# Performance work log

Hardware: AMD Instinct MI355X
Metric: run time of the kernel (lower is better)

Reference implementation:

```python
import jax, jax.numpy as jnp
import numpy as np

N, L, D_MODEL, N_HEADS = 2, 2048, 512, 8

def setup_inputs() -> dict:
    key = jax.random.key(0)
    x = jax.random.normal(key, (N, L, D_MODEL), dtype=jnp.float32)
    return {"input_data": x}

def reference(input_data):
    n, l, _ = input_data.shape
    h = N_HEADS
    d = D_MODEL // h  # head dim
    # Q = K = V = reshaped input (the Linear projections are unused in the original forward)
    q = input_data.reshape(n, l, h, d)
    k = q
    v = q
    scale = 1.0 / jnp.sqrt(jnp.float32(d))
    # scores: [n, h, l, s]
    scores = jnp.einsum('nlhd,nshd->nhls', q, k)
    attn_weights = jax.nn.softmax(scale * scores, axis=-1)
    # updated values: [n, l, h, d]
    updated_v = jnp.einsum('nhls,nshd->nlhd', attn_weights, v)
    out = updated_v.reshape(n, l, h * d)
    # attn returned as mean over heads: permute nhls -> nlhs, mean over h -> [n, l, s]
    attn = jnp.transpose(attn_weights, (0, 2, 1, 3)).mean(axis=-2)
    return (out, attn)
```

## Files before the change

### kernel.cpp

```cpp
#include <hip/hip_runtime.h>

#define NBATCH 2
#define SEQ    2048
#define DMODEL 512
#define NH     8
#define HDIM   64
#define SCALE  0.125f

typedef __attribute__((ext_vector_type(8))) short bf16x8;
typedef __attribute__((ext_vector_type(4))) float f32x4;

__device__ __forceinline__ unsigned short f2bf(float f) {
    union { float f; unsigned u; } v; v.f = f;
    unsigned r = v.u + 0x7FFFu + ((v.u >> 16) & 1u);
    return (unsigned short)(r >> 16);
}

__device__ __forceinline__ void pack4(unsigned short* dst, float4 v) {
    unsigned long long pk = (unsigned long long)f2bf(v.x)
        | ((unsigned long long)f2bf(v.y) << 16)
        | ((unsigned long long)f2bf(v.z) << 32)
        | ((unsigned long long)f2bf(v.w) << 48);
    *(unsigned long long*)dst = pk;
}

__device__ __forceinline__ bf16x8 pack8(float4 a, float4 b) {
    bf16x8 r;
    r[0]=(short)f2bf(a.x); r[1]=(short)f2bf(a.y); r[2]=(short)f2bf(a.z); r[3]=(short)f2bf(a.w);
    r[4]=(short)f2bf(b.x); r[5]=(short)f2bf(b.y); r[6]=(short)f2bf(b.z); r[7]=(short)f2bf(b.w);
    return r;
}

__device__ __forceinline__ void gld_lds16(const unsigned short* g, unsigned short* l) {
    __builtin_amdgcn_global_load_lds(
        (const __attribute__((address_space(1))) unsigned int*)(const void*)g,
        (__attribute__((address_space(3))) unsigned int*)(void*)l, 16, 0, 0);
}

__global__ __launch_bounds__(256) void prep_kernel(const float* __restrict__ x,
                                                   unsigned short* __restrict__ xb,
                                                   unsigned short* __restrict__ xt) {
    __shared__ unsigned short Tb[64][72];
    const int bid = blockIdx.x;
    const int n = bid >> 8, h = (bid >> 5) & 7, st = bid & 31;
    const int s0 = st * 64;
    const int t = threadIdx.x;
    {
        const int s = t >> 2, d0 = (t & 3) * 16;
        const float* xp = x + ((size_t)(n*SEQ + s0 + s))*DMODEL + h*HDIM + d0;
        #pragma unroll
        for (int i = 0; i < 4; ++i) pack4(&Tb[s][d0 + 4*i], *(const float4*)(xp + 4*i));
    }
    __syncthreads();
    {
        const int s = t >> 2, d0 = (t & 3) * 16;
        unsigned short* bp = xb + ((size_t)(n*SEQ + s0 + s))*DMODEL + h*HDIM + d0;
        *(bf16x8*)bp       = *(const bf16x8*)&Tb[s][d0];
        *(bf16x8*)(bp + 8) = *(const bf16x8*)&Tb[s][d0 + 8];
    }
    {
        const int d = t >> 2, c0 = (t & 3) * 16;
        bf16x8 v0, v1;
        #pragma unroll
        for (int j = 0; j < 8; ++j) {
            v0[j] = (short)Tb[c0 + j][d];
            v1[j] = (short)Tb[c0 + 8 + j][d];
        }
        unsigned short* tp = xt + ((size_t)((n*NH + h)*HDIM + d))*SEQ + s0 + c0;
        *(bf16x8*)tp       = v0;
        *(bf16x8*)(tp + 8) = v1;
    }
}

__global__ __launch_bounds__(256) void out_kernel3(const unsigned short* __restrict__ xb,
                                                   const unsigned short* __restrict__ xt,
                                                   float* __restrict__ out,
                                                   float* __restrict__ rho) {
    __shared__ unsigned short Kb[2][64*64];
    __shared__ unsigned short Vt[2][64*64];
    __shared__ unsigned short pb[64][72];

    const int i   = blockIdx.x;
    const int bid = (i & 7) * 64 + (i >> 3);
    const int n = bid >> 8, h = (bid >> 5) & 7, lt = bid & 31;
    const int l0 = lt * 64;
    const int tid = threadIdx.x;
    const int wv = tid >> 6, lane = tid & 63;
    const int lr = lane & 15, lg = lane >> 4;

    const unsigned short* qp = xb + ((size_t)(n*SEQ + l0 + wv*16 + lr))*DMODEL + h*HDIM + lg*8;
    const bf16x8 a0 = *(const bf16x8*)qp;
    const bf16x8 a1 = *(const bf16x8*)(qp + 32);

    const int srow8  = wv*8 + (lane >> 3);
    const int schunk = lane & 7;
    const unsigned short* kbase = xb + (size_t)(n*SEQ)*DMODEL + h*HDIM;
    const unsigned short* vbase = xt + ((size_t)(n*NH + h)*HDIM)*SEQ;

    auto stage = [&](int buf, int s0) {
        #pragma unroll
        for (int it = 0; it < 2; ++it) {
            const int row = it*32 + srow8;
            const int gc  = schunk ^ (row & 7);
            gld_lds16(kbase + (size_t)(s0 + row)*DMODEL + gc*8,
                      &Kb[buf][it*2048 + wv*512]);
        }
        #pragma unroll
        for (int it = 0; it < 2; ++it) {
            const int d  = it*32 + srow8;
            const int gc = schunk ^ (d & 7);
            gld_lds16(vbase + (size_t)d*SEQ + s0 + gc*8,
                      &Vt[buf][it*2048 + wv*512]);
        }
    };

    f32x4 ov0 = {0.f,0.f,0.f,0.f}, ov1 = {0.f,0.f,0.f,0.f};
    f32x4 ov2 = {0.f,0.f,0.f,0.f}, ov3 = {0.f,0.f,0.f,0.f};
    float rs[4] = {0.f,0.f,0.f,0.f};

    stage(0, 0);
    __syncthreads();
    int cur = 0;

    for (int c = 0; c < 32; ++c) {
        if (c < 31) stage(cur ^ 1, (c + 1) * 64);

        const int c0 = (lg ^ (lr & 7)) << 3;
        #pragma unroll
        for (int ct = 0; ct < 4; ++ct) {
            const unsigned short* kr = &Kb[cur][(ct*16 + lr)*64];
            bf16x8 b0 = *(const bf16x8*)&kr[c0];
            bf16x8 b1 = *(const bf16x8*)&kr[c0 ^ 32];
            f32x4 acc = {0.f,0.f,0.f,0.f};
            acc = __builtin_amdgcn_mfma_f32_16x16x32_bf16(a0, b0, acc, 0,0,0);
            acc = __builtin_amdgcn_mfma_f32_16x16x32_bf16(a1, b1, acc, 0,0,0);
            #pragma unroll
            for (int r = 0; r < 4; ++r) {
                const float e = __expf(acc[r] * SCALE);
                rs[r] += e;
                pb[wv*16 + lg*4 + r][ct*16 + lr] = f2bf(e);
            }
        }
        #pragma unroll
        for (int ks = 0; ks < 2; ++ks) {
            const bf16x8 pa = *(const bf16x8*)&pb[wv*16 + lr][ks*32 + lg*8];
            const int cc = ((ks*4 + lg) ^ (lr & 7)) << 3;
            const bf16x8 w0 = *(const bf16x8*)&Vt[cur][( 0 + lr)*64 + cc];
            const bf16x8 w1 = *(const bf16x8*)&Vt[cur][(16 + lr)*64 + cc];
            const bf16x8 w2 = *(const bf16x8*)&Vt[cur][(32 + lr)*64 + cc];
            const bf16x8 w3 = *(const bf16x8*)&Vt[cur][(48 + lr)*64 + cc];
            ov0 = __builtin_amdgcn_mfma_f32_16x16x32_bf16(pa, w0, ov0, 0,0,0);
            ov1 = __builtin_amdgcn_mfma_f32_16x16x32_bf16(pa, w1, ov1, 0,0,0);
            ov2 = __builtin_amdgcn_mfma_f32_16x16x32_bf16(pa, w2, ov2, 0,0,0);
            ov3 = __builtin_amdgcn_mfma_f32_16x16x32_bf16(pa, w3, ov3, 0,0,0);
        }
        __syncthreads();
        cur ^= 1;
    }

    #pragma unroll
    for (int r = 0; r < 4; ++r) {
        float s = rs[r];
        s += __shfl_xor(s, 1, 16);
        s += __shfl_xor(s, 2, 16);
        s += __shfl_xor(s, 4, 16);
        s += __shfl_xor(s, 8, 16);
        rs[r] = s;
    }
    const int row0 = l0 + wv*16 + lg*4;
    if (lr == 0) {
        #pragma unroll
        for (int r = 0; r < 4; ++r)
            rho[(size_t)(n*NH + h)*SEQ + row0 + r] = rs[r];
    }
    #pragma unroll
    for (int r = 0; r < 4; ++r) {
        const float iv = 1.f / rs[r];
        float* op = out + ((size_t)(n*SEQ + row0 + r))*DMODEL + h*HDIM + lr;
        op[0]  = ov0[r] * iv;
        op[16] = ov1[r] * iv;
        op[32] = ov2[r] * iv;
        op[48] = ov3[r] * iv;
    }
}

__global__ __launch_bounds__(256) void mean_kernel3(const unsigned short* __restrict__ xb,
                                                    const float* __restrict__ rho,
                                                    float* __restrict__ attn) {
    __shared__ unsigned short Qb[2][64*64];
    __shared__ unsigned short Kb[2][64*64];
    __shared__ float invb[NH][64];

    const int i   = blockIdx.x;
    const int bid = (i & 7) * 256 + (i >> 3);
    const int n = bid >> 10, lt = (bid >> 5) & 31, st = bid & 31;
    const int l0 = lt * 64, s0 = st * 64;
    const int tid = threadIdx.x;
    const int wv = tid >> 6, lane = tid & 63;
    const int lr = lane & 15, lg = lane >> 4;

    for (int j = tid; j < NH*64; j += 256) {
        const int hh = j >> 6, row = j & 63;
        invb[hh][row] = 0.125f / rho[(size_t)(n*NH + hh)*SEQ + l0 + row];
    }

    const int srow8  = wv*8 + (lane >> 3);
    const int schunk = lane & 7;

    auto stage = [&](int buf, int h) {
        #pragma unroll
        for (int it = 0; it < 2; ++it) {
            const int row = it*32 + srow8;
            const int gc  = schunk ^ (row & 7);
            gld_lds16(xb + ((size_t)(n*SEQ + l0 + row))*DMODEL + h*HDIM + gc*8,
                      &Qb[buf][it*2048 + wv*512]);
        }
        #pragma unroll
        for (int it = 0; it < 2; ++it) {
            const int row = it*32 + srow8;
            const int gc  = schunk ^ (row & 7);
            gld_lds16(xb + ((size_t)(n*SEQ + s0 + row))*DMODEL + h*HDIM + gc*8,
                      &Kb[buf][it*2048 + wv*512]);
        }
    };

    float mean[4][4];
    #pragma unroll
    for (int ct = 0; ct < 4; ++ct)
        #pragma unroll
        for (int r = 0; r < 4; ++r) mean[ct][r] = 0.f;

    stage(0, 0);
    __syncthreads();
    int cur = 0;

    for (int h = 0; h < NH; ++h) {
        if (h < NH-1) stage(cur ^ 1, h + 1);

        const int qrow = wv*16 + lr;
        const int c0 = (lg ^ (lr & 7)) << 3;
        const bf16x8 a0 = *(const bf16x8*)&Qb[cur][qrow*64 + c0];
        const bf16x8 a1 = *(const bf16x8*)&Qb[cur][qrow*64 + (c0 ^ 32)];
        #pragma unroll
        for (int ct = 0; ct < 4; ++ct) {
            const unsigned short* kr = &Kb[cur][(ct*16 + lr)*64];
            bf16x8 b0 = *(const bf16x8*)&kr[c0];
            bf16x8 b1 = *(const bf16x8*)&kr[c0 ^ 32];
            f32x4 acc = {0.f,0.f,0.f,0.f};
            acc = __builtin_amdgcn_mfma_f32_16x16x32_bf16(a0, b0, acc, 0,0,0);
            acc = __builtin_amdgcn_mfma_f32_16x16x32_bf16(a1, b1, acc, 0,0,0);
            #pragma unroll
            for (int r = 0; r < 4; ++r)
                mean[ct][r] += __expf(acc[r] * SCALE) * invb[h][wv*16 + lg*4 + r];
        }
        __syncthreads();
        cur ^= 1;
    }

    #pragma unroll
    for (int ct = 0; ct < 4; ++ct)
        #pragma unroll
        for (int r = 0; r < 4; ++r)
            attn[((size_t)(n*SEQ + l0 + wv*16 + lg*4 + r))*SEQ + s0 + ct*16 + lr]
                = mean[ct][r];
}

__global__ __launch_bounds__(256) void fb_out_kernel(const float* __restrict__ x,
                                                     float* __restrict__ out,
                                                     float* __restrict__ rho) {
    __shared__ unsigned short Kbuf[128][72];
    __shared__ unsigned short vT[64][136];
    __shared__ unsigned short pbuf[64][136];
    const int bid = blockIdx.x;
    const int n  = bid >> 8, h = (bid >> 5) & 7, lt = bid & 31;
    const int l0 = lt * 64;
    const int tid = threadIdx.x;
    const int wv  = tid >> 6, lane = tid & 63;
    const int lr  = lane & 15, lg = lane >> 4;
    const float* qp = x + ((size_t)(n*SEQ + l0 + wv*16 + lr))*DMODEL + h*HDIM + lg*8;
    const bf16x8 a0 = pack8(*(const float4*)qp,      *(const float4*)(qp+4));
    const bf16x8 a1 = pack8(*(const float4*)(qp+32), *(const float4*)(qp+36));
    f32x4 ov0 = {0.f,0.f,0.f,0.f}, ov1 = {0.f,0.f,0.f,0.f};
    f32x4 ov2 = {0.f,0.f,0.f,0.f}, ov3 = {0.f,0.f,0.f,0.f};
    float rs[4] = {0.f,0.f,0.f,0.f};
    for (int s0 = 0; s0 < SEQ; s0 += 128) {
        __syncthreads();
        {
            const int srow = tid >> 1, dbase = (tid & 1) * 32;
            const float* kp = x + ((size_t)(n*SEQ + s0 + srow))*DMODEL + h*HDIM + dbase;
            #pragma unroll
            for (int i = 0; i < 8; ++i) {
                float4 v = *(const float4*)(kp + 4*i);
                pack4(&Kbuf[srow][dbase + 4*i], v);
                const int d = dbase + 4*i;
                vT[d+0][srow] = f2bf(v.x); vT[d+1][srow] = f2bf(v.y);
                vT[d+2][srow] = f2bf(v.z); vT[d+3][srow] = f2bf(v.w);
            }
        }
        __syncthreads();
        #pragma unroll
        for (int ct = 0; ct < 8; ++ct) {
            const unsigned short* bp = &Kbuf[ct*16 + lr][lg*8];
            bf16x8 b0 = *(const bf16x8*)bp;
            bf16x8 b1 = *(const bf16x8*)(bp + 32);
            f32x4 acc = {0.f,0.f,0.f,0.f};
            acc = __builtin_amdgcn_mfma_f32_16x16x32_bf16(a0, b0, acc, 0,0,0);
            acc = __builtin_amdgcn_mfma_f32_16x16x32_bf16(a1, b1, acc, 0,0,0);
            #pragma unroll
            for (int r = 0; r < 4; ++r) {
                const float e = __expf(acc[r] * SCALE);
                rs[r] += e;
                pbuf[wv*16 + lg*4 + r][ct*16 + lr] = f2bf(e);
            }
        }
        __syncthreads();
        #pragma unroll
        for (int ks = 0; ks < 4; ++ks) {
            bf16x8 pa = *(const bf16x8*)&pbuf[wv*16 + lr][ks*32 + lg*8];
            bf16x8 v0 = *(const bf16x8*)&vT[ 0 + lr][ks*32 + lg*8];
            bf16x8 v1 = *(const bf16x8*)&vT[16 + lr][ks*32 + lg*8];
            bf16x8 v2 = *(const bf16x8*)&vT[32 + lr][ks*32 + lg*8];
            bf16x8 v3 = *(const bf16x8*)&vT[48 + lr][ks*32 + lg*8];
            ov0 = __builtin_amdgcn_mfma_f32_16x16x32_bf16(pa, v0, ov0, 0,0,0);
            ov1 = __builtin_amdgcn_mfma_f32_16x16x32_bf16(pa, v1, ov1, 0,0,0);
            ov2 = __builtin_amdgcn_mfma_f32_16x16x32_bf16(pa, v2, ov2, 0,0,0);
            ov3 = __builtin_amdgcn_mfma_f32_16x16x32_bf16(pa, v3, ov3, 0,0,0);
        }
    }
    #pragma unroll
    for (int r = 0; r < 4; ++r) {
        float s = rs[r];
        s += __shfl_xor(s, 1, 16); s += __shfl_xor(s, 2, 16);
        s += __shfl_xor(s, 4, 16); s += __shfl_xor(s, 8, 16);
        rs[r] = s;
    }
    const int row0 = l0 + wv*16 + lg*4;
    if (lr == 0) {
        #pragma unroll
        for (int r = 0; r < 4; ++r)
            rho[(size_t)(n*NH + h)*SEQ + row0 + r] = rs[r];
    }
    #pragma unroll
    for (int r = 0; r < 4; ++r) {
        const float iv = 1.f / rs[r];
        float* op = out + ((size_t)(n*SEQ + row0 + r))*DMODEL + h*HDIM + lr;
        op[0] = ov0[r]*iv; op[16] = ov1[r]*iv; op[32] = ov2[r]*iv; op[48] = ov3[r]*iv;
    }
}

__global__ __launch_bounds__(256) void fb_mean_kernel(const float* __restrict__ x,
                                                      const float* __restrict__ rho,
                                                      float* __restrict__ attn) {
    __shared__ unsigned short Qb[64][72];
    __shared__ unsigned short Kb[128][72];
    __shared__ float          invb[64];
    const int bid = blockIdx.x;
    const int n  = bid >> 9, lt = (bid >> 4) & 31, st = bid & 15;
    const int l0 = lt * 64, s0 = st * 128;
    const int tid = threadIdx.x;
    const int wv  = tid >> 6, lane = tid & 63;
    const int lr  = lane & 15, lg = lane >> 4;
    float mean[8][4];
    #pragma unroll
    for (int ct = 0; ct < 8; ++ct)
        #pragma unroll
        for (int r = 0; r < 4; ++r) mean[ct][r] = 0.f;
    for (int h = 0; h < NH; ++h) {
        __syncthreads();
        {
            const int qrow = tid >> 2, qd = (tid & 3) * 16;
            const float* qp = x + ((size_t)(n*SEQ + l0 + qrow))*DMODEL + h*HDIM + qd;
            #pragma unroll
            for (int i = 0; i < 4; ++i)
                pack4(&Qb[qrow][qd + 4*i], *(const float4*)(qp + 4*i));
        }
        {
            const int srow = tid >> 1, dbase = (tid & 1) * 32;
            const float* kp = x + ((size_t)(n*SEQ + s0 + srow))*DMODEL + h*HDIM + dbase;
            #pragma unroll
            for (int i = 0; i < 8; ++i)
                pack4(&Kb[srow][dbase + 4*i], *(const float4*)(kp + 4*i));
        }
        if (tid < 64)
            invb[tid] = 0.125f / rho[(size_t)(n*NH + h)*SEQ + l0 + tid];
        __syncthreads();
        const unsigned short* ap = &Qb[wv*16 + lr][lg*8];
        const bf16x8 a0 = *(const bf16x8*)ap;
        const bf16x8 a1 = *(const bf16x8*)(ap + 32);
        #pragma unroll
        for (int ct = 0; ct < 8; ++ct) {
            const unsigned short* bp = &Kb[ct*16 + lr][lg*8];
            bf16x8 b0 = *(const bf16x8*)bp;
            bf16x8 b1 = *(const bf16x8*)(bp + 32);
            f32x4 acc = {0.f,0.f,0.f,0.f};
            acc = __builtin_amdgcn_mfma_f32_16x16x32_bf16(a0, b0, acc, 0,0,0);
            acc = __builtin_amdgcn_mfma_f32_16x16x32_bf16(a1, b1, acc, 0,0,0);
            #pragma unroll
            for (int r = 0; r < 4; ++r)
                mean[ct][r] += __expf(acc[r] * SCALE) * invb[wv*16 + lg*4 + r];
        }
    }
    #pragma unroll
    for (int ct = 0; ct < 8; ++ct)
        #pragma unroll
        for (int r = 0; r < 4; ++r)
            attn[((size_t)(n*SEQ + l0 + wv*16 + lg*4 + r))*SEQ + s0 + ct*16 + lr]
                = mean[ct][r];
}

extern "C" void kernel_launch(void* const* d_in, const int* in_sizes, int n_in,
                              void* d_out, int out_size, void* d_ws, size_t ws_size,
                              hipStream_t stream) {
    (void)in_sizes; (void)n_in; (void)out_size;
    const float* x = (const float*)d_in[0];
    float* out  = (float*)d_out;
    float* attn = out + (size_t)NBATCH*SEQ*DMODEL;
    float* rho  = (float*)d_ws;

    const size_t XB_OFF = 131072;
    const size_t XT_OFF = XB_OFF + 4194304;
    const size_t NEED   = XT_OFF + 4194304;

    if (ws_size >= NEED) {
        unsigned short* xb = (unsigned short*)((char*)d_ws + XB_OFF);
        unsigned short* xt = (unsigned short*)((char*)d_ws + XT_OFF);
        prep_kernel <<<dim3(512),  dim3(256), 0, stream>>>(x, xb, xt);
        out_kernel3 <<<dim3(512),  dim3(256), 0, stream>>>(xb, xt, out, rho);
        mean_kernel3<<<dim3(2048), dim3(256), 0, stream>>>(xb, rho, attn);
    } else {
        fb_out_kernel <<<dim3(512),  dim3(256), 0, stream>>>(x, out, rho);
        fb_mean_kernel<<<dim3(1024), dim3(256), 0, stream>>>(x, rho, attn);
    }
}
```

Baseline: 89.56 us.

## Transpose MFMA scores, use exp2 with folded scale, MFMA row sums, vector attn stores

Swaps the MFMA operands so each lane holds four consecutive key columns of one query row. This allows packed 8-byte P writes to LDS and float4 stores of the attention mean. Exponentials now use exp2 with the scale and log2(e) folded into one constant, and the per-row 1/rho factor is moved into the exponent via log2. Row sums are computed by an extra MFMA against a ones vector instead of scalar accumulation and shuffles. The row sum now comes from bf16-rounded probabilities, which slightly changes normalisation accuracy.

Measured after the change: 81.68 us. 1.1x faster.

```diff
diff --git a/kernel.cpp b/kernel.cpp
--- a/kernel.cpp
+++ b/kernel.cpp
@@ -7,6 +7,14 @@
 #define HDIM   64
 #define SCALE  0.125f
 
+#define K2 0.1803368801111204f
+
+#if __has_builtin(__builtin_amdgcn_exp2f)
+#define EXP2(x) __builtin_amdgcn_exp2f(x)
+#else
+#define EXP2(x) __expf((x) * 0.6931471805599453f)
+#endif
+
 typedef __attribute__((ext_vector_type(8))) short bf16x8;
 typedef __attribute__((ext_vector_type(4))) float f32x4;
 
@@ -21,7 +29,7 @@
         | ((unsigned long long)f2bf(v.y) << 16)
         | ((unsigned long long)f2bf(v.z) << 32)
         | ((unsigned long long)f2bf(v.w) << 48);
-    *(unsigned long long*)dst = pk;
+    __builtin_memcpy(dst, &pk, 8);
 }
 
 __device__ __forceinline__ bf16x8 pack8(float4 a, float4 b) {
@@ -72,7 +80,7 @@
     }
 }
 
-__global__ __launch_bounds__(256) void out_kernel3(const unsigned short* __restrict__ xb,
+__global__ __launch_bounds__(256) void out_kernel4(const unsigned short* __restrict__ xb,
                                                    const unsigned short* __restrict__ xt,
                                                    float* __restrict__ out,
                                                    float* __restrict__ rho) {
@@ -92,6 +100,10 @@
     const bf16x8 a0 = *(const bf16x8*)qp;
     const bf16x8 a1 = *(const bf16x8*)(qp + 32);
 
+    bf16x8 ones;
+    #pragma unroll
+    for (int j = 0; j < 8; ++j) ones[j] = (short)0x3F80;
+
     const int srow8  = wv*8 + (lane >> 3);
     const int schunk = lane & 7;
     const unsigned short* kbase = xb + (size_t)(n*SEQ)*DMODEL + h*HDIM;
@@ -116,7 +128,7 @@
 
     f32x4 ov0 = {0.f,0.f,0.f,0.f}, ov1 = {0.f,0.f,0.f,0.f};
     f32x4 ov2 = {0.f,0.f,0.f,0.f}, ov3 = {0.f,0.f,0.f,0.f};
-    float rs[4] = {0.f,0.f,0.f,0.f};
+    f32x4 ovS = {0.f,0.f,0.f,0.f};
 
     stage(0, 0);
     __syncthreads();
@@ -132,14 +144,17 @@
             bf16x8 b0 = *(const bf16x8*)&kr[c0];
             bf16x8 b1 = *(const bf16x8*)&kr[c0 ^ 32];
             f32x4 acc = {0.f,0.f,0.f,0.f};
-            acc = __builtin_amdgcn_mfma_f32_16x16x32_bf16(a0, b0, acc, 0,0,0);
-            acc = __builtin_amdgcn_mfma_f32_16x16x32_bf16(a1, b1, acc, 0,0,0);
-            #pragma unroll
-            for (int r = 0; r < 4; ++r) {
-                const float e = __expf(acc[r] * SCALE);
-                rs[r] += e;
-                pb[wv*16 + lg*4 + r][ct*16 + lr] = f2bf(e);
-            }
+            acc = __builtin_amdgcn_mfma_f32_16x16x32_bf16(b0, a0, acc, 0,0,0);
+            acc = __builtin_amdgcn_mfma_f32_16x16x32_bf16(b1, a1, acc, 0,0,0);
+            const float e0 = EXP2(acc[0] * K2);
+            const float e1 = EXP2(acc[1] * K2);
+            const float e2 = EXP2(acc[2] * K2);
+            const float e3 = EXP2(acc[3] * K2);
+            unsigned long long pk = (unsigned long long)f2bf(e0)
+                | ((unsigned long long)f2bf(e1) << 16)
+                | ((unsigned long long)f2bf(e2) << 32)
+                | ((unsigned long long)f2bf(e3) << 48);
+            __builtin_memcpy(&pb[wv*16 + lr][ct*16 + lg*4], &pk, 8);
         }
         #pragma unroll
         for (int ks = 0; ks < 2; ++ks) {
@@ -153,29 +168,21 @@
             ov1 = __builtin_amdgcn_mfma_f32_16x16x32_bf16(pa, w1, ov1, 0,0,0);
             ov2 = __builtin_amdgcn_mfma_f32_16x16x32_bf16(pa, w2, ov2, 0,0,0);
             ov3 = __builtin_amdgcn_mfma_f32_16x16x32_bf16(pa, w3, ov3, 0,0,0);
+            ovS = __builtin_amdgcn_mfma_f32_16x16x32_bf16(pa, ones, ovS, 0,0,0);
         }
         __syncthreads();
         cur ^= 1;
     }
 
-    #pragma unroll
-    for (int r = 0; r < 4; ++r) {
-        float s = rs[r];
-        s += __shfl_xor(s, 1, 16);
-        s += __shfl_xor(s, 2, 16);
-        s += __shfl_xor(s, 4, 16);
-        s += __shfl_xor(s, 8, 16);
-        rs[r] = s;
-    }
     const int row0 = l0 + wv*16 + lg*4;
     if (lr == 0) {
         #pragma unroll
         for (int r = 0; r < 4; ++r)
-            rho[(size_t)(n*NH + h)*SEQ + row0 + r] = rs[r];
+            rho[(size_t)(n*NH + h)*SEQ + row0 + r] = ovS[r];
     }
     #pragma unroll
     for (int r = 0; r < 4; ++r) {
-        const float iv = 1.f / rs[r];
+        const float iv = 1.f / ovS[r];
         float* op = out + ((size_t)(n*SEQ + row0 + r))*DMODEL + h*HDIM + lr;
         op[0]  = ov0[r] * iv;
         op[16] = ov1[r] * iv;
@@ -184,7 +191,7 @@
     }
 }
 
-__global__ __launch_bounds__(256) void mean_kernel3(const unsigned short* __restrict__ xb,
+__global__ __launch_bounds__(256) void mean_kernel4(const unsigned short* __restrict__ xb,
                                                     const float* __restrict__ rho,
                                                     float* __restrict__ attn) {
     __shared__ unsigned short Qb[2][64*64];
@@ -241,28 +248,29 @@
         const int c0 = (lg ^ (lr & 7)) << 3;
         const bf16x8 a0 = *(const bf16x8*)&Qb[cur][qrow*64 + c0];
         const bf16x8 a1 = *(const bf16x8*)&Qb[cur][qrow*64 + (c0 ^ 32)];
+        const float logiv = __log2f(invb[h][wv*16 + lr]);
         #pragma unroll
         for (int ct = 0; ct < 4; ++ct) {
             const unsigned short* kr = &Kb[cur][(ct*16 + lr)*64];
             bf16x8 b0 = *(const bf16x8*)&kr[c0];
             bf16x8 b1 = *(const bf16x8*)&kr[c0 ^ 32];
             f32x4 acc = {0.f,0.f,0.f,0.f};
-            acc = __builtin_amdgcn_mfma_f32_16x16x32_bf16(a0, b0, acc, 0,0,0);
-            acc = __builtin_amdgcn_mfma_f32_16x16x32_bf16(a1, b1, acc, 0,0,0);
+            acc = __builtin_amdgcn_mfma_f32_16x16x32_bf16(b0, a0, acc, 0,0,0);
+            acc = __builtin_amdgcn_mfma_f32_16x16x32_bf16(b1, a1, acc, 0,0,0);
             #pragma unroll
             for (int r = 0; r < 4; ++r)
-                mean[ct][r] += __expf(acc[r] * SCALE) * invb[h][wv*16 + lg*4 + r];
+                mean[ct][r] += EXP2(fmaf(acc[r], K2, logiv));
         }
         __syncthreads();
         cur ^= 1;
     }
 
-    #pragma unroll
-    for (int ct = 0; ct < 4; ++ct)
-        #pragma unroll
-        for (int r = 0; r < 4; ++r)
-            attn[((size_t)(n*SEQ + l0 + wv*16 + lg*4 + r))*SEQ + s0 + ct*16 + lr]
-                = mean[ct][r];
+    const int arow = n*SEQ + l0 + wv*16 + lr;
+    #pragma unroll
+    for (int ct = 0; ct < 4; ++ct) {
+        float4 v = { mean[ct][0], mean[ct][1], mean[ct][2], mean[ct][3] };
+        *(float4*)&attn[(size_t)arow*SEQ + s0 + ct*16 + lg*4] = v;
+    }
 }
 
 __global__ __launch_bounds__(256) void fb_out_kernel(const float* __restrict__ x,
@@ -425,8 +433,8 @@
         unsigned short* xb = (unsigned short*)((char*)d_ws + XB_OFF);
         unsigned short* xt = (unsigned short*)((char*)d_ws + XT_OFF);
         prep_kernel <<<dim3(512),  dim3(256), 0, stream>>>(x, xb, xt);
-        out_kernel3 <<<dim3(512),  dim3(256), 0, stream>>>(xb, xt, out, rho);
-        mean_kernel3<<<dim3(2048), dim3(256), 0, stream>>>(xb, rho, attn);
+        out_kernel4 <<<dim3(512),  dim3(256), 0, stream>>>(xb, xt, out, rho);
+        mean_kernel4<<<dim3(2048), dim3(256), 0, stream>>>(xb, rho, attn);
     } else {
         fb_out_kernel <<<dim3(512),  dim3(256), 0, stream>>>(x, out, rho);
         fb_mean_kernel<<<dim3(1024), dim3(256), 0, stream>>>(x, rho, attn);
```
